# Performance work log

Measured on AMD Instinct MI355X. Metric: run time of the kernel, lower is better.

Reference implementation:

```python
import jax, jax.numpy as jnp
import numpy as np
from jax import lax

B, T, F_IN = 16, 512, 229
CONV = 768      # model_complexity_conv * 16
LSTM_H = 768    # model_complexity_lstm * 16
P = 88          # output_features
NCLS = 5
EMB = 2


def _conv(x, w, b, pad):
    y = lax.conv_general_dilated(x, w, (1, 1), pad,
                                 dimension_numbers=('NCHW', 'OIHW', 'NCHW'))
    return y + b[None, :, None, None]


def _bn(x, g, bta, m, v):
    # eval-mode BatchNorm2d with running stats, eps=1e-5
    s = g * lax.rsqrt(v + 1e-5)
    return x * s[None, :, None, None] + (bta - m * s)[None, :, None, None]


def _pool2w(x):
    # MaxPool2d((1,2))
    return lax.reduce_window(x, -jnp.inf, lax.max, (1, 1, 1, 2), (1, 1, 1, 2), 'VALID')


def _cell(x, h, c, Wih, Whh, bih, bhh):
    # PyTorch LSTM cell, gate order i,f,g,o
    z = x @ Wih.T + h @ Whh.T + bih + bhh
    i, f, g, o = jnp.split(z, 4, axis=-1)
    c = jax.nn.sigmoid(f) * c + jax.nn.sigmoid(i) * jnp.tanh(g)
    h = jax.nn.sigmoid(o) * jnp.tanh(c)
    return h, c


def _forward(mel, c1w, c1b, bn1g, bn1b, bn1m, bn1v,
             c2w, c2b, bn2g, bn2b, bn2m, bn2v,
             c3w, c3b, bn3g, bn3b, bn3m, bn3v,
             fcw, fcb, wih0, whh0, bih0, bhh0,
             wih1, whh1, bih1, bhh1, pw, pb, emb):
    # ---- ConvStack (eval mode: dropout = identity) ----
    x = mel[:, None]                                   # (B,1,T,F)
    x = jax.nn.relu(_bn(_conv(x, c1w, c1b, [(1, 1), (1, 1)]), bn1g, bn1b, bn1m, bn1v))
    x = jax.nn.relu(_bn(_conv(x, c2w, c2b, [(1, 1), (1, 1)]), bn2g, bn2b, bn2m, bn2v))
    x = _pool2w(x)
    x = jax.nn.relu(_bn(_conv(x, c3w, c3b, [(0, 0), (1, 1)]), bn3g, bn3b, bn3m, bn3v))  # time -2
    x = _pool2w(x)                                     # (B, C/8, T-2, F//4)
    x = jnp.transpose(x, (0, 2, 1, 3)).reshape(x.shape[0], x.shape[2], -1)
    acoustic = x @ fcw.T + fcb                         # (B, T-2, CONV)

    Bsz = acoustic.shape[0]
    h1 = jnp.zeros((Bsz, LSTM_H), acoustic.dtype)
    c1 = jnp.zeros((Bsz, LSTM_H), acoustic.dtype)
    h2 = jnp.zeros((Bsz, LSTM_H), acoustic.dtype)
    c2 = jnp.zeros((Bsz, LSTM_H), acoustic.dtype)
    prev = jnp.zeros((Bsz, P * EMB), acoustic.dtype)

    def step(carry, a_t):
        h1, c1, h2, c2, prev = carry
        xt = jnp.concatenate([a_t, prev], axis=-1)     # (B, CONV + 2P)
        h1, c1 = _cell(xt, h1, c1, wih0, whh0, bih0, bhh0)
        h2, c2 = _cell(h1, h2, c2, wih1, whh1, bih1, bhh1)
        logits = (h2 @ pw.T + pb).reshape(Bsz, P, NCLS)
        idx = jnp.argmax(logits, axis=-1)              # argmax(softmax) == argmax(logits)
        prev = emb[idx].reshape(Bsz, P * EMB)
        return (h1, c1, h2, c2, prev), logits

    _, out = lax.scan(step, (h1, c1, h2, c2, prev), jnp.swapaxes(acoustic, 0, 1))
    return jnp.swapaxes(out, 0, 1)                     # (B, T-2, P, 5) raw logits


def setup_inputs() -> dict:
    key = jax.random.key(0)
    ks = iter(jax.random.split(key, 48))

    def rn(shape, s=0.05):
        return jax.random.normal(next(ks), shape, dtype=jnp.float32) * s

    C16, C8 = CONV // 16, CONV // 8
    d = {}
    d['mel'] = jax.random.normal(next(ks), (B, T, F_IN), dtype=jnp.float32)
    d['c1w'] = rn((C16, 1, 3, 3), 0.2); d['c1b'] = rn((C16,))
    d['c2w'] = rn((C16, C16, 3, 3), 0.1); d['c2b'] = rn((C16,))
    d['c3w'] = rn((C8, C16, 3, 3), 0.1); d['c3b'] = rn((C8,))
    for n, ch in (('1', C16), ('2', C16), ('3', C8)):
        d['bn%sg' % n] = jnp.ones((ch,), jnp.float32)
        d['bn%sb' % n] = jnp.zeros((ch,), jnp.float32)
        d['bn%sm' % n] = rn((ch,), 0.1)
        d['bn%sv' % n] = jnp.ones((ch,), jnp.float32)
    d['fcw'] = rn((CONV, C8 * (F_IN // 4)), 0.02); d['fcb'] = rn((CONV,))
    in_l = CONV + P * EMB
    d['wih0'] = rn((4 * LSTM_H, in_l), 0.03); d['whh0'] = rn((4 * LSTM_H, LSTM_H), 0.03)
    d['bih0'] = rn((4 * LSTM_H,)); d['bhh0'] = rn((4 * LSTM_H,))
    d['wih1'] = rn((4 * LSTM_H, LSTM_H), 0.03); d['whh1'] = rn((4 * LSTM_H, LSTM_H), 0.03)
    d['bih1'] = rn((4 * LSTM_H,)); d['bhh1'] = rn((4 * LSTM_H,))
    d['pw'] = rn((P * NCLS, LSTM_H), 0.03); d['pb'] = rn((P * NCLS,))
    d['emb'] = rn((NCLS, EMB), 1.0)
    return d


def reference(mel, c1w, c1b, c2w, c2b, c3w, c3b,
              bn1g, bn1b, bn1m, bn1v, bn2g, bn2b, bn2m, bn2v,
              bn3g, bn3b, bn3m, bn3v, fcw, fcb,
              wih0, whh0, bih0, bhh0, wih1, whh1, bih1, bhh1,
              pw, pb, emb):
    return _forward(mel, c1w, c1b, bn1g, bn1b, bn1m, bn1v,
                    c2w, c2b, bn2g, bn2b, bn2m, bn2v,
                    c3w, c3b, bn3g, bn3b, bn3m, bn3v,
                    fcw, fcb, wih0, whh0, bih0, bhh0,
                    wih1, whh1, bih1, bhh1, pw, pb, emb)
```

## Files before the change

### kernel.cpp

```cpp
#include <hip/hip_runtime.h>
#include <math.h>


typedef unsigned long long ull;

#define ACO_FL 6266880ull
#define F1_OFF 0
#define F2_OFF 3072
#define PC_OFF 6144
#define BAR_U32 8192
#define NCOMP 192
#define NPROJ 44

__device__ __forceinline__ float sigf(float x) { return 1.0f / (1.0f + expf(-x)); }

__device__ __forceinline__ ull pack2(float x, float y) {
  union { float f[2]; ull u; } c; c.f[0] = x; c.f[1] = y; return c.u;
}
__device__ __forceinline__ ull at_load(const ull* p) {
  return __hip_atomic_load((ull*)p, __ATOMIC_RELAXED, __HIP_MEMORY_SCOPE_AGENT);
}
__device__ __forceinline__ void at_store(ull* p, ull v) {
  __hip_atomic_store(p, v, __ATOMIC_RELAXED, __HIP_MEMORY_SCOPE_AGENT);
}

__device__ __forceinline__ void gl2lds(const float4* g, float* l) {
  __builtin_amdgcn_global_load_lds(
      (const __attribute__((address_space(1))) void*)(g),
      (__attribute__((address_space(3))) void*)(l), 16, 0, 17);
}
__device__ __forceinline__ void gl2lds_nc(const float4* g, float* l) {
  __builtin_amdgcn_global_load_lds(
      (const __attribute__((address_space(1))) void*)(g),
      (__attribute__((address_space(3))) void*)(l), 16, 0, 0);
}

__device__ __forceinline__ void wait_flags(const unsigned* f, unsigned tgt, int tid) {
  if (tid < NCOMP) {
    const unsigned* fp = f + tid * 16;
    while (__hip_atomic_load((unsigned*)fp, __ATOMIC_RELAXED,
                             __HIP_MEMORY_SCOPE_AGENT) < tgt)
      __builtin_amdgcn_s_sleep(1);
  }
  __atomic_signal_fence(__ATOMIC_SEQ_CST);
  __syncthreads();
}

__device__ __forceinline__ void pwait(const unsigned* pc, unsigned target) {
  for (;;) {
    unsigned s0 = 0;
#pragma unroll
    for (int i = 0; i < 8; ++i)
      s0 += __hip_atomic_load((unsigned*)(pc + i * 16), __ATOMIC_RELAXED,
                              __HIP_MEMORY_SCOPE_AGENT);
    if (s0 >= target) break;
    __builtin_amdgcn_s_sleep(1);
  }
  __atomic_signal_fence(__ATOMIC_SEQ_CST);
}

__device__ __forceinline__ float red16(float v) {
  v += __shfl_xor(v, 1, 16);
  v += __shfl_xor(v, 2, 16);
  v += __shfl_xor(v, 4, 16);
  v += __shfl_xor(v, 8, 16);
  return v;
}

#define CDOT48(W, PTR, RES) do {                                              \
  const float* _p = (PTR);                                                    \
  float _a0 = 0.f, _a1 = 0.f, _a2 = 0.f, _a3 = 0.f;                           \
  _Pragma("unroll")                                                           \
  for (int _i = 0; _i < 48; _i += 16) {                                       \
    float4 _v0 = *(const float4*)(_p + _i);                                   \
    float4 _v1 = *(const float4*)(_p + _i + 4);                               \
    float4 _v2 = *(const float4*)(_p + _i + 8);                               \
    float4 _v3 = *(const float4*)(_p + _i + 12);                              \
    _a0 = fmaf((W)[_i + 0], _v0.x, _a0); _a0 = fmaf((W)[_i + 1], _v0.y, _a0); \
    _a0 = fmaf((W)[_i + 2], _v0.z, _a0); _a0 = fmaf((W)[_i + 3], _v0.w, _a0); \
    _a1 = fmaf((W)[_i + 4], _v1.x, _a1); _a1 = fmaf((W)[_i + 5], _v1.y, _a1); \
    _a1 = fmaf((W)[_i + 6], _v1.z, _a1); _a1 = fmaf((W)[_i + 7], _v1.w, _a1); \
    _a2 = fmaf((W)[_i + 8], _v2.x, _a2); _a2 = fmaf((W)[_i + 9], _v2.y, _a2); \
    _a2 = fmaf((W)[_i +10], _v2.z, _a2); _a2 = fmaf((W)[_i +11], _v2.w, _a2); \
    _a3 = fmaf((W)[_i +12], _v3.x, _a3); _a3 = fmaf((W)[_i +13], _v3.y, _a3); \
    _a3 = fmaf((W)[_i +14], _v3.z, _a3); _a3 = fmaf((W)[_i +15], _v3.w, _a3); \
  }                                                                           \
  RES = (_a0 + _a1) + (_a2 + _a3);                                            \
} while (0)

#define STAGE_H(SRC, DSTF) do {                                              \
  const float4* _g = (const float4*)(const void*)(SRC);                      \
  _Pragma("unroll")                                                          \
  for (int _cc = 0; _cc < 4; ++_cc) {                                        \
    int _c = wv * 4 + _cc;                                                   \
    _Pragma("unroll")                                                        \
    for (int _k = 0; _k < 3; ++_k)                                           \
      gl2lds(_g + _c * 192 + _k * 64 + ln, (DSTF) + _c * 772 + _k * 256);    \
  }                                                                          \
} while (0)

#define STAGE_PREV(PAR) do {                                                 \
  const float4* _gp = (const float4*)(const void*)(prevg + (size_t)(PAR) * 1408); \
  _Pragma("unroll")                                                          \
  for (int _j = 0; _j < 11; ++_j)                                            \
    if (wv == (_j & 3))                                                      \
      gl2lds(_gp + _j * 64 + ln, prevs + _j * 256);                          \
} while (0)

#define STAGE_X(T) do {                                                      \
  const float4* _gx = (const float4*)(aco + (size_t)(T) * 12288);            \
  _Pragma("unroll")                                                          \
  for (int _cc = 0; _cc < 4; ++_cc) {                                        \
    int _c = wv * 4 + _cc;                                                   \
    _Pragma("unroll")                                                        \
    for (int _k = 0; _k < 3; ++_k) {                                         \
      int _u = _k * 64 + ln;                                                 \
      int _b = _u / 12, _m = _u - _b * 12;                                   \
      gl2lds_nc(_gx + _b * 192 + _c * 12 + _m, bufA + _c * 772 + _k * 256);  \
    }                                                                        \
  }                                                                          \
} while (0)

__global__ __launch_bounds__(256) void conv12_kernel(
    const float* __restrict__ mel,
    const float* __restrict__ c1w, const float* __restrict__ c1b,
    const float* __restrict__ bn1g, const float* __restrict__ bn1b,
    const float* __restrict__ bn1m, const float* __restrict__ bn1v,
    const float* __restrict__ c2w, const float* __restrict__ c2b,
    const float* __restrict__ bn2g, const float* __restrict__ bn2b,
    const float* __restrict__ bn2m, const float* __restrict__ bn2v,
    float* __restrict__ A, int b0)
{
  __shared__ float melS[5 * 232];
  __shared__ float x1S[12 * 3 * 232];
  __shared__ float wS[48 * 12 * 9];
  const int tid = threadIdx.x;
  const int bl = blockIdx.x >> 9;
  const int b = b0 + bl;
  const int t = blockIdx.x & 511;

  for (int idx = tid; idx < 5 * 232; idx += 256) {
    int rr = idx / 232, cc = idx - rr * 232;
    int r = t - 2 + rr, w = cc - 1;
    float v = 0.f;
    if (r >= 0 && r < 512 && w >= 0 && w < 229) v = mel[(b * 512 + r) * 229 + w];
    melS[idx] = v;
  }

  float accA[22], accB[22];
#pragma unroll
  for (int i = 0; i < 22; ++i) { accA[i] = 0.f; accB[i] = 0.f; }
  __syncthreads();

  for (int icc = 0; icc < 4; ++icc) {
    if (icc) __syncthreads();
    for (int idx = tid; idx < 12 * 3 * 232; idx += 256) {
      int cl = idx / (3 * 232);
      int rem = idx - cl * (3 * 232);
      int rr = rem / 232, cc = rem - rr * 232;
      int c = icc * 12 + cl;
      int r1 = t - 1 + rr, w = cc - 1;
      float v = 0.f;
      if (r1 >= 0 && r1 < 512 && w >= 0 && w < 229) {
        const float* cw = c1w + c * 9;
        const float* m0 = melS + rr * 232 + cc - 1;
        float s = m0[0] * cw[0] + m0[1] * cw[1] + m0[2] * cw[2]
                + m0[232] * cw[3] + m0[233] * cw[4] + m0[234] * cw[5]
                + m0[464] * cw[6] + m0[465] * cw[7] + m0[466] * cw[8];
        s += c1b[c];
        float sc = bn1g[c] * rsqrtf(bn1v[c] + 1e-5f);
        v = fmaxf(s * sc + (bn1b[c] - bn1m[c] * sc), 0.f);
      }
      x1S[idx] = v;
    }
    for (int idx = tid; idx < 48 * 12 * 9; idx += 256) {
      int oc = idx / 108, rem = idx - oc * 108;
      wS[idx] = c2w[(oc * 48 + icc * 12) * 9 + rem];
    }
    __syncthreads();
    for (int i = 0; i < 22; ++i) {
      int oidx = tid + i * 256;
      if (oidx >= 5472) break;
      int oc = oidx / 114, wp = oidx - oc * 114;
      int w0 = 2 * wp;
      float a0 = accA[i], a1 = accB[i];
      const float* wp9 = wS + oc * 108;
      for (int icl = 0; icl < 12; ++icl) {
#pragma unroll
        for (int a = 0; a < 3; ++a) {
          const float* xr = x1S + (icl * 3 + a) * 232 + w0;
          float x0 = xr[0], x1 = xr[1], x2 = xr[2], x3 = xr[3];
          float wA = wp9[icl * 9 + a * 3 + 0];
          float wB = wp9[icl * 9 + a * 3 + 1];
          float wC = wp9[icl * 9 + a * 3 + 2];
          a0 = fmaf(x0, wA, a0); a0 = fmaf(x1, wB, a0); a0 = fmaf(x2, wC, a0);
          a1 = fmaf(x1, wA, a1); a1 = fmaf(x2, wB, a1); a1 = fmaf(x3, wC, a1);
        }
      }
      accA[i] = a0; accB[i] = a1;
    }
  }
  for (int i = 0; i < 22; ++i) {
    int oidx = tid + i * 256;
    if (oidx >= 5472) break;
    int oc = oidx / 114, wp = oidx - oc * 114;
    float sc = bn2g[oc] * rsqrtf(bn2v[oc] + 1e-5f);
    float sh = bn2b[oc] - bn2m[oc] * sc;
    float v0 = fmaxf((accA[i] + c2b[oc]) * sc + sh, 0.f);
    float v1 = fmaxf((accB[i] + c2b[oc]) * sc + sh, 0.f);
    A[((bl * 48 + oc) * 512 + t) * 114 + wp] = fmaxf(v0, v1);
  }
}

__global__ __launch_bounds__(256) void conv3_kernel(
    const float* __restrict__ A,
    const float* __restrict__ c3w, const float* __restrict__ c3b,
    const float* __restrict__ bn3g, const float* __restrict__ bn3b,
    const float* __restrict__ bn3m, const float* __restrict__ bn3v,
    float* __restrict__ Bf)
{
  __shared__ float aS[16 * 3 * 116];
  __shared__ float wS[48 * 16 * 9];
  const int tid = threadIdx.x;
  const int bl = blockIdx.x / 510;
  const int t = blockIdx.x - bl * 510;

  for (int ocg = 0; ocg < 2; ++ocg) {
    float accA[11], accB[11];
#pragma unroll
    for (int i = 0; i < 11; ++i) { accA[i] = 0.f; accB[i] = 0.f; }
    for (int icc = 0; icc < 3; ++icc) {
      __syncthreads();
      for (int idx = tid; idx < 16 * 3 * 116; idx += 256) {
        int cl = idx / 348, rem = idx - cl * 348;
        int rr = rem / 116, cc = rem - rr * 116;
        int w = cc - 1;
        float v = 0.f;
        if (w >= 0 && w < 114) v = A[((bl * 48 + icc * 16 + cl) * 512 + t + rr) * 114 + w];
        aS[idx] = v;
      }
      for (int idx = tid; idx < 48 * 16 * 9; idx += 256) {
        int ocl = idx / 144, rem = idx - ocl * 144;
        wS[idx] = c3w[((ocg * 48 + ocl) * 48 + icc * 16) * 9 + rem];
      }
      __syncthreads();
      for (int i = 0; i < 11; ++i) {
        int oidx = tid + i * 256;
        if (oidx >= 2736) break;
        int ocl = oidx / 57, wp = oidx - ocl * 57;
        int w0 = 2 * wp;
        float a0 = accA[i], a1 = accB[i];
        const float* wb = wS + ocl * 144;
        for (int icl = 0; icl < 16; ++icl) {
#pragma unroll
          for (int a = 0; a < 3; ++a) {
            const float* xr = aS + (icl * 3 + a) * 116 + w0;
            float x0 = xr[0], x1 = xr[1], x2 = xr[2], x3 = xr[3];
            float wA = wb[icl * 9 + a * 3 + 0];
            float wB = wb[icl * 9 + a * 3 + 1];
            float wC = wb[icl * 9 + a * 3 + 2];
            a0 = fmaf(x0, wA, a0); a0 = fmaf(x1, wB, a0); a0 = fmaf(x2, wC, a0);
            a1 = fmaf(x1, wA, a1); a1 = fmaf(x2, wB, a1); a1 = fmaf(x3, wC, a1);
          }
        }
        accA[i] = a0; accB[i] = a1;
      }
    }
    for (int i = 0; i < 11; ++i) {
      int oidx = tid + i * 256;
      if (oidx >= 2736) break;
      int ocl = oidx / 57, wp = oidx - ocl * 57;
      int oc = ocg * 48 + ocl;
      float sc = bn3g[oc] * rsqrtf(bn3v[oc] + 1e-5f);
      float sh = bn3b[oc] - bn3m[oc] * sc;
      float v0 = fmaxf((accA[i] + c3b[oc]) * sc + sh, 0.f);
      float v1 = fmaxf((accB[i] + c3b[oc]) * sc + sh, 0.f);
      Bf[(size_t)(bl * 510 + t) * 5472 + oc * 57 + wp] = fmaxf(v0, v1);
    }
  }
}

__global__ __launch_bounds__(256) void gemm_nt(
    const float* __restrict__ Am, const float* __restrict__ Bm,
    const float* __restrict__ bias, float* __restrict__ C,
    int M, int K, int lda, int ldb, int b0)
{
  __shared__ float As[64 * 33];
  __shared__ float Bs[64 * 33];
  const int tid = threadIdx.x;
  const int m0 = blockIdx.x * 64, n0 = blockIdx.y * 64;
  const int tx = tid & 15, ty = tid >> 4;
  const int kq = (tid & 7) * 4, rw = tid >> 3;
  float acc[4][4];
#pragma unroll
  for (int i = 0; i < 4; ++i)
#pragma unroll
    for (int j = 0; j < 4; ++j) acc[i][j] = 0.f;

  for (int k0 = 0; k0 < K; k0 += 32) {
    int m1 = m0 + rw, m2 = m1 + 32;
    float4 va = make_float4(0.f, 0.f, 0.f, 0.f), vb = va;
    if (m1 < M) va = *(const float4*)(Am + (size_t)m1 * lda + k0 + kq);
    if (m2 < M) vb = *(const float4*)(Am + (size_t)m2 * lda + k0 + kq);
    float4 wa = *(const float4*)(Bm + (size_t)(n0 + rw) * ldb + k0 + kq);
    float4 wb = *(const float4*)(Bm + (size_t)(n0 + rw + 32) * ldb + k0 + kq);
    As[rw * 33 + kq + 0] = va.x; As[rw * 33 + kq + 1] = va.y;
    As[rw * 33 + kq + 2] = va.z; As[rw * 33 + kq + 3] = va.w;
    As[(rw + 32) * 33 + kq + 0] = vb.x; As[(rw + 32) * 33 + kq + 1] = vb.y;
    As[(rw + 32) * 33 + kq + 2] = vb.z; As[(rw + 32) * 33 + kq + 3] = vb.w;
    Bs[rw * 33 + kq + 0] = wa.x; Bs[rw * 33 + kq + 1] = wa.y;
    Bs[rw * 33 + kq + 2] = wa.z; Bs[rw * 33 + kq + 3] = wa.w;
    Bs[(rw + 32) * 33 + kq + 0] = wb.x; Bs[(rw + 32) * 33 + kq + 1] = wb.y;
    Bs[(rw + 32) * 33 + kq + 2] = wb.z; Bs[(rw + 32) * 33 + kq + 3] = wb.w;
    __syncthreads();
#pragma unroll 8
    for (int k = 0; k < 32; ++k) {
      float av[4], bv[4];
#pragma unroll
      for (int i = 0; i < 4; ++i) av[i] = As[(ty * 4 + i) * 33 + k];
#pragma unroll
      for (int j = 0; j < 4; ++j) bv[j] = Bs[(tx * 4 + j) * 33 + k];
#pragma unroll
      for (int i = 0; i < 4; ++i)
#pragma unroll
        for (int j = 0; j < 4; ++j) acc[i][j] = fmaf(av[i], bv[j], acc[i][j]);
    }
    __syncthreads();
  }
#pragma unroll
  for (int i = 0; i < 4; ++i) {
    int m = m0 + ty * 4 + i;
    if (m >= M) continue;
    int bl2 = m / 510, tt2 = m - bl2 * 510;
    float* crow = C + ((size_t)tt2 * 16 + (b0 + bl2)) * 768;
#pragma unroll
    for (int j = 0; j < 4; ++j) {
      int n = n0 + tx * 4 + j;
      crow[n] = acc[i][j] + bias[n];
    }
  }
}

__global__ void init_state(ull* __restrict__ h1g, ull* __restrict__ h2g,
                           ull* __restrict__ prevg, unsigned* __restrict__ bar) {
  int gid = blockIdx.x * 256 + threadIdx.x;
  if (gid < 12288) { at_store(h1g + gid, 0ull); at_store(h2g + gid, 0ull); }
  if (gid < 2816) at_store(prevg + gid, 0ull);
  if (gid < BAR_U32)
    __hip_atomic_store(bar + gid, 0u, __ATOMIC_RELAXED, __HIP_MEMORY_SCOPE_AGENT);
}

__global__ __launch_bounds__(256, 1) void lstm_kernel(
    const float* __restrict__ aco,
    const float* __restrict__ whh0,
    const float* __restrict__ wih0,
    const float* __restrict__ wih1,
    const float* __restrict__ whh1,
    const float* __restrict__ bih0, const float* __restrict__ bhh0,
    const float* __restrict__ bih1, const float* __restrict__ bhh1,
    const float* __restrict__ pw,
    const float* __restrict__ pb,
    const float* __restrict__ emb,
    ull* __restrict__ h1g,
    ull* __restrict__ h2g,
    ull* __restrict__ prevg,
    unsigned* __restrict__ bar,
    float* __restrict__ out)
{
  __shared__ float bufA[16 * 772];
  __shared__ float bufB[16 * 772];
  __shared__ float bufC[16 * 772];
  __shared__ float prevs[16 * 176];
  __shared__ float zl[16 * 17];
  __shared__ float harr[64];
  __shared__ float embS[10];
  const int tid = threadIdx.x;
  const int s = tid & 15;
  const int r = tid >> 4;
  const int wv = tid >> 6;
  const int ln = tid & 63;
  unsigned* f1 = bar + F1_OFF;
  unsigned* f2 = bar + F2_OFF;
  unsigned* pc = bar + PC_OFF;

  if (blockIdx.x < NCOMP) {
    const int uB = blockIdx.x * 4;
    const int j = (r >> 2) * 768 + uB + (r & 3);

    float wx[48], w0[48], w1[48], w2[48], wp[11];
    {
      const float* p = wih0 + (size_t)j * 944 + 48 * s;
#pragma unroll
      for (int i = 0; i < 48; i += 4) {
        float4 v = *(const float4*)(p + i);
        wx[i] = v.x; wx[i+1] = v.y; wx[i+2] = v.z; wx[i+3] = v.w;
      }
      p = whh0 + (size_t)j * 768 + 48 * s;
#pragma unroll
      for (int i = 0; i < 48; i += 4) {
        float4 v = *(const float4*)(p + i);
        w0[i] = v.x; w0[i+1] = v.y; w0[i+2] = v.z; w0[i+3] = v.w;
      }
      p = wih1 + (size_t)j * 768 + 48 * s;
#pragma unroll
      for (int i = 0; i < 48; i += 4) {
        float4 v = *(const float4*)(p + i);
        w1[i] = v.x; w1[i+1] = v.y; w1[i+2] = v.z; w1[i+3] = v.w;
      }
      p = whh1 + (size_t)j * 768 + 48 * s;
#pragma unroll
      for (int i = 0; i < 48; i += 4) {
        float4 v = *(const float4*)(p + i);
        w2[i] = v.x; w2[i+1] = v.y; w2[i+2] = v.z; w2[i+3] = v.w;
      }
      const float* pp = wih0 + (size_t)j * 944 + 768 + 11 * s;
#pragma unroll
      for (int i = 0; i < 11; ++i) wp[i] = pp[i];
    }
    float bl1[4], bl2[4], c1 = 0.f, c2 = 0.f;
    if (tid < 64) {
      int ul = tid >> 4;
#pragma unroll
      for (int g = 0; g < 4; ++g) {
        int jj = g * 768 + uB + ul;
        bl1[g] = bih0[jj] + bhh0[jj];
        bl2[g] = bih1[jj] + bhh1[jj];
      }
    }
    const int hdst = (blockIdx.x / 12) * 384 + (blockIdx.x % 12) * 2;

    for (int i = tid; i < 16 * 772; i += 256) { bufB[i] = 0.f; bufC[i] = 0.f; }

    float zxr[16];
    STAGE_X(0);
    __syncthreads();
#pragma unroll 4
    for (int b = 0; b < 16; ++b) {
      float p; CDOT48(wx, bufA + s * 772 + b * 48, p);
      zxr[b] = red16(p);
    }

    for (int t = 0; t < 510; ++t) {
      const int wbuf = t & 1, rbuf = wbuf ^ 1;
      __syncthreads();
#pragma unroll 4
      for (int b = 0; b < 16; ++b) {
        float p; CDOT48(w0, bufB + s * 772 + b * 48, p);
        p = red16(p);
        if (s == 0) zl[r * 17 + b] = zxr[b] + p;
      }
      if (tid == 0 && t) pwait(pc, (unsigned)(NPROJ * t));
      __syncthreads();
      STAGE_H(h2g + rbuf * 6144, bufC);
      STAGE_PREV(rbuf);
      __syncthreads();
#pragma unroll 4
      for (int b = 0; b < 16; ++b) {
        const float* pvv = prevs + b * 176 + s * 11;
        float p = 0.f;
#pragma unroll
        for (int i = 0; i < 11; ++i) p = fmaf(wp[i], pvv[i], p);
        p = red16(p);
        if (s == 0) zl[r * 17 + b] += p;
      }
      __syncthreads();
      if (tid < 64) {
        int ul = tid >> 4, bb = tid & 15;
        float zi = zl[(0 * 4 + ul) * 17 + bb] + bl1[0];
        float zf = zl[(1 * 4 + ul) * 17 + bb] + bl1[1];
        float zg = zl[(2 * 4 + ul) * 17 + bb] + bl1[2];
        float zo = zl[(3 * 4 + ul) * 17 + bb] + bl1[3];
        c1 = sigf(zf) * c1 + sigf(zi) * tanhf(zg);
        harr[tid] = sigf(zo) * tanhf(c1);
      }
      __syncthreads();
      if (tid < 32) {
        int q = tid >> 4, bb = tid & 15;
        at_store(h1g + wbuf * 6144 + hdst + bb * 24 + q,
                 pack2(harr[(2 * q) * 16 + bb], harr[(2 * q + 1) * 16 + bb]));
      }
      if (tid == 0) {
        __builtin_amdgcn_s_waitcnt(0);
        __atomic_signal_fence(__ATOMIC_SEQ_CST);
        __hip_atomic_store(f1 + blockIdx.x * 16, (unsigned)(t + 1),
                           __ATOMIC_RELAXED, __HIP_MEMORY_SCOPE_AGENT);
      }
      if (t < 509) {
        STAGE_X(t + 1);
        __syncthreads();
#pragma unroll 4
        for (int b = 0; b < 16; ++b) {
          float p; CDOT48(wx, bufA + s * 772 + b * 48, p);
          zxr[b] = red16(p);
        }
      }
      wait_flags(f1, (unsigned)(t + 1), tid);
      STAGE_H(h1g + wbuf * 6144, bufB);
      __syncthreads();
#pragma unroll 2
      for (int b = 0; b < 16; ++b) {
        float p1, p2;
        CDOT48(w1, bufB + s * 772 + b * 48, p1);
        CDOT48(w2, bufC + s * 772 + b * 48, p2);
        float p = red16(p1 + p2);
        if (s == 0) zl[r * 17 + b] = p;
      }
      __syncthreads();
      if (tid < 64) {
        int ul = tid >> 4, bb = tid & 15;
        float zi = zl[(0 * 4 + ul) * 17 + bb] + bl2[0];
        float zf = zl[(1 * 4 + ul) * 17 + bb] + bl2[1];
        float zg = zl[(2 * 4 + ul) * 17 + bb] + bl2[2];
        float zo = zl[(3 * 4 + ul) * 17 + bb] + bl2[3];
        c2 = sigf(zf) * c2 + sigf(zi) * tanhf(zg);
        harr[tid] = sigf(zo) * tanhf(c2);
      }
      __syncthreads();
      if (tid < 32) {
        int q = tid >> 4, bb = tid & 15;
        at_store(h2g + wbuf * 6144 + hdst + bb * 24 + q,
                 pack2(harr[(2 * q) * 16 + bb], harr[(2 * q + 1) * 16 + bb]));
      }
      if (tid == 0) {
        __builtin_amdgcn_s_waitcnt(0);
        __atomic_signal_fence(__ATOMIC_SEQ_CST);
        __hip_atomic_store(f2 + blockIdx.x * 16, (unsigned)(t + 1),
                           __ATOMIC_RELAXED, __HIP_MEMORY_SCOPE_AGENT);
      }
    }
  } else {
    const int bp = blockIdx.x - NCOMP;
    const int prow = bp * 10 + r;
    float pwr[48];
    float pbv = 0.f;
    if (r < 10) {
      const float* p = pw + (size_t)prow * 768 + 48 * s;
#pragma unroll
      for (int i = 0; i < 48; i += 4) {
        float4 v = *(const float4*)(p + i);
        pwr[i] = v.x; pwr[i+1] = v.y; pwr[i+2] = v.z; pwr[i+3] = v.w;
      }
      pbv = pb[prow];
    } else {
#pragma unroll
      for (int i = 0; i < 48; ++i) pwr[i] = 0.f;
    }
    if (tid < 10) embS[tid] = emb[tid];
    __syncthreads();

    for (int t = 0; t < 510; ++t) {
      const int wbuf = t & 1;
      wait_flags(f2, (unsigned)(t + 1), tid);
      STAGE_H(h2g + wbuf * 6144, bufA);
      __syncthreads();
#pragma unroll 4
      for (int b = 0; b < 16; ++b) {
        float p; CDOT48(pwr, bufA + s * 772 + b * 48, p);
        p = red16(p);
        if (r < 10 && s == 0) {
          float lg = p + pbv;
          out[((size_t)b * 510 + t) * 440 + prow] = lg;
          zl[r * 17 + b] = lg;
        }
      }
      __syncthreads();
      if (tid < 32) {
        int q = tid >> 4, bb = tid & 15;
        float best = zl[(q * 5) * 17 + bb]; int bi = 0;
#pragma unroll
        for (int c = 1; c < 5; ++c) {
          float v = zl[(q * 5 + c) * 17 + bb];
          if (v > best) { best = v; bi = c; }
        }
        at_store(prevg + wbuf * 1408 + bb * 88 + bp * 2 + q,
                 pack2(embS[bi * 2], embS[bi * 2 + 1]));
      }
      __syncthreads();
      if (tid == 0) {
        __builtin_amdgcn_s_waitcnt(0);
        __atomic_signal_fence(__ATOMIC_SEQ_CST);
        __hip_atomic_fetch_add(pc + (bp & 7) * 16, 1u,
                               __ATOMIC_RELAXED, __HIP_MEMORY_SCOPE_AGENT);
      }
    }
  }
}

extern "C" void kernel_launch(void* const* d_in, const int* in_sizes, int n_in,
                              void* d_out, int out_size, void* d_ws, size_t ws_size,
                              hipStream_t stream) {
  (void)in_sizes; (void)n_in; (void)out_size;
  const float* mel  = (const float*)d_in[0];
  const float* c1w  = (const float*)d_in[1];
  const float* c1b  = (const float*)d_in[2];
  const float* c2w  = (const float*)d_in[3];
  const float* c2b  = (const float*)d_in[4];
  const float* c3w  = (const float*)d_in[5];
  const float* c3b  = (const float*)d_in[6];
  const float* bn1g = (const float*)d_in[7];
  const float* bn1b = (const float*)d_in[8];
  const float* bn1m = (const float*)d_in[9];
  const float* bn1v = (const float*)d_in[10];
  const float* bn2g = (const float*)d_in[11];
  const float* bn2b = (const float*)d_in[12];
  const float* bn2m = (const float*)d_in[13];
  const float* bn2v = (const float*)d_in[14];
  const float* bn3g = (const float*)d_in[15];
  const float* bn3b = (const float*)d_in[16];
  const float* bn3m = (const float*)d_in[17];
  const float* bn3v = (const float*)d_in[18];
  const float* fcw  = (const float*)d_in[19];
  const float* fcb  = (const float*)d_in[20];
  const float* wih0 = (const float*)d_in[21];
  const float* whh0 = (const float*)d_in[22];
  const float* bih0 = (const float*)d_in[23];
  const float* bhh0 = (const float*)d_in[24];
  const float* wih1 = (const float*)d_in[25];
  const float* whh1 = (const float*)d_in[26];
  const float* bih1 = (const float*)d_in[27];
  const float* bhh1 = (const float*)d_in[28];
  const float* pw   = (const float*)d_in[29];
  const float* pb   = (const float*)d_in[30];
  const float* emb  = (const float*)d_in[31];

  float* ws = (float*)d_ws;
  float* outp = (float*)d_out;

  const size_t ST_ULL = 12288ull + 12288ull + 2816ull;
  int CB = 1;
  for (int cb = 4; cb >= 1; cb >>= 1) {
    size_t need = (ACO_FL + (size_t)cb * 48 * 512 * 114 + (size_t)cb * 510 * 5472) * 4
                + ST_ULL * 8 + BAR_U32 * 4 + 1024;
    if (ws_size >= need) { CB = cb; break; }
  }
  const int nchunks = 16 / CB;
  const size_t A_FL  = (size_t)CB * 48 * 512 * 114;
  const size_t BF_FL = (size_t)CB * 510 * 5472;

  float* aco = ws;
  float* Ac  = ws + ACO_FL;
  float* Bfc = Ac + A_FL;
  ull* h1g   = (ull*)(Bfc + BF_FL);
  ull* h2g   = h1g + 12288;
  ull* prevg = h2g + 12288;
  unsigned* bar = (unsigned*)(prevg + 2816);

  for (int ch = 0; ch < nchunks; ++ch) {
    int b0 = ch * CB;
    hipLaunchKernelGGL(conv12_kernel, dim3(CB * 512), dim3(256), 0, stream,
                       mel, c1w, c1b, bn1g, bn1b, bn1m, bn1v,
                       c2w, c2b, bn2g, bn2b, bn2m, bn2v, Ac, b0);
    hipLaunchKernelGGL(conv3_kernel, dim3(CB * 510), dim3(256), 0, stream,
                       Ac, c3w, c3b, bn3g, bn3b, bn3m, bn3v, Bfc);
    int M = CB * 510;
    hipLaunchKernelGGL(gemm_nt, dim3((M + 63) / 64, 12), dim3(256), 0, stream,
                       Bfc, fcw, fcb, aco, M, 5472, 5472, 5472, b0);
  }
  hipLaunchKernelGGL(init_state, dim3(48), dim3(256), 0, stream,
                     h1g, h2g, prevg, bar);

  {
    void* args[] = {
      (void*)&aco, (void*)&whh0, (void*)&wih0, (void*)&wih1, (void*)&whh1,
      (void*)&bih0, (void*)&bhh0, (void*)&bih1, (void*)&bhh1,
      (void*)&pw, (void*)&pb, (void*)&emb,
      (void*)&h1g, (void*)&h2g, (void*)&prevg, (void*)&bar, (void*)&outp
    };
    hipError_t e = hipLaunchCooperativeKernel((const void*)lstm_kernel,
                                              dim3(NCOMP + NPROJ), dim3(256),
                                              args, 0, stream);
    if (e != hipSuccess) {
      (void)hipGetLastError();
      hipLaunchKernelGGL(lstm_kernel, dim3(NCOMP + NPROJ), dim3(256), 0, stream,
                         aco, whh0, wih0, wih1, whh1, bih0, bhh0, bih1, bhh1,
                         pw, pb, emb, h1g, h2g, prevg, bar, outp);
    }
  }
}
```

Before: 25.84 ms.

## Replace projection counter barrier with per-block flags and trim syncthreads

The projection blocks now each publish their own step counter, and the compute blocks poll these flags in parallel across threads instead of one thread summing eight atomically incremented counters. The gate outputs are exchanged by wavefront shuffles rather than through a shared array, which removes a block barrier per layer. The next-step x staging is issued earlier so it overlaps the recurrent dot products, and the sleep interval while polling goes from 1 to 4. The changes aim to shorten the per-timestep critical path of the 510-step serial decode. They also relax ordering: one barrier in the projection blocks is dropped, and the earlier staging of x writes into bufA, so correctness depends on the remaining barriers still ordering those accesses.

Result: faster. 24.84 ms (-3.9%).

```diff
diff --git a/kernel.cpp b/kernel.cpp
--- a/kernel.cpp
+++ b/kernel.cpp
@@ -7,7 +7,7 @@
 #define ACO_FL 6266880ull
 #define F1_OFF 0
 #define F2_OFF 3072
-#define PC_OFF 6144
+#define FP_OFF 6144
 #define BAR_U32 8192
 #define NCOMP 192
 #define NPROJ 44
@@ -35,28 +35,20 @@
       (__attribute__((address_space(3))) void*)(l), 16, 0, 0);
 }
 
-__device__ __forceinline__ void wait_flags(const unsigned* f, unsigned tgt, int tid) {
-  if (tid < NCOMP) {
+__device__ __forceinline__ void wait_flags_n(const unsigned* f, unsigned tgt,
+                                             int tid, int n) {
+  if (tid < n) {
     const unsigned* fp = f + tid * 16;
-    while (__hip_atomic_load((unsigned*)fp, __ATOMIC_RELAXED,
-                             __HIP_MEMORY_SCOPE_AGENT) < tgt)
-      __builtin_amdgcn_s_sleep(1);
+    unsigned v = __hip_atomic_load((unsigned*)fp, __ATOMIC_RELAXED,
+                                   __HIP_MEMORY_SCOPE_AGENT);
+    while (v < tgt) {
+      __builtin_amdgcn_s_sleep(4);
+      v = __hip_atomic_load((unsigned*)fp, __ATOMIC_RELAXED,
+                            __HIP_MEMORY_SCOPE_AGENT);
+    }
   }
   __atomic_signal_fence(__ATOMIC_SEQ_CST);
   __syncthreads();
-}
-
-__device__ __forceinline__ void pwait(const unsigned* pc, unsigned target) {
-  for (;;) {
-    unsigned s0 = 0;
-#pragma unroll
-    for (int i = 0; i < 8; ++i)
-      s0 += __hip_atomic_load((unsigned*)(pc + i * 16), __ATOMIC_RELAXED,
-                              __HIP_MEMORY_SCOPE_AGENT);
-    if (s0 >= target) break;
-    __builtin_amdgcn_s_sleep(1);
-  }
-  __atomic_signal_fence(__ATOMIC_SEQ_CST);
 }
 
 __device__ __forceinline__ float red16(float v) {
@@ -372,7 +364,6 @@
   __shared__ float bufC[16 * 772];
   __shared__ float prevs[16 * 176];
   __shared__ float zl[16 * 17];
-  __shared__ float harr[64];
   __shared__ float embS[10];
   const int tid = threadIdx.x;
   const int s = tid & 15;
@@ -381,7 +372,7 @@
   const int ln = tid & 63;
   unsigned* f1 = bar + F1_OFF;
   unsigned* f2 = bar + F2_OFF;
-  unsigned* pc = bar + PC_OFF;
+  unsigned* fp = bar + FP_OFF;
 
   if (blockIdx.x < NCOMP) {
     const int uB = blockIdx.x * 4;
@@ -443,14 +434,15 @@
     for (int t = 0; t < 510; ++t) {
       const int wbuf = t & 1, rbuf = wbuf ^ 1;
       __syncthreads();
+      if (t < 509) STAGE_X(t + 1);
 #pragma unroll 4
       for (int b = 0; b < 16; ++b) {
         float p; CDOT48(w0, bufB + s * 772 + b * 48, p);
         p = red16(p);
         if (s == 0) zl[r * 17 + b] = zxr[b] + p;
       }
-      if (tid == 0 && t) pwait(pc, (unsigned)(NPROJ * t));
-      __syncthreads();
+      if (t) wait_flags_n(fp, (unsigned)t, tid, NPROJ);
+      else __syncthreads();
       STAGE_H(h2g + rbuf * 6144, bufC);
       STAGE_PREV(rbuf);
       __syncthreads();
@@ -471,30 +463,29 @@
         float zg = zl[(2 * 4 + ul) * 17 + bb] + bl1[2];
         float zo = zl[(3 * 4 + ul) * 17 + bb] + bl1[3];
         c1 = sigf(zf) * c1 + sigf(zi) * tanhf(zg);
-        harr[tid] = sigf(zo) * tanhf(c1);
-      }
-      __syncthreads();
-      if (tid < 32) {
-        int q = tid >> 4, bb = tid & 15;
-        at_store(h1g + wbuf * 6144 + hdst + bb * 24 + q,
-                 pack2(harr[(2 * q) * 16 + bb], harr[(2 * q + 1) * 16 + bb]));
-      }
-      if (tid == 0) {
-        __builtin_amdgcn_s_waitcnt(0);
-        __atomic_signal_fence(__ATOMIC_SEQ_CST);
-        __hip_atomic_store(f1 + blockIdx.x * 16, (unsigned)(t + 1),
-                           __ATOMIC_RELAXED, __HIP_MEMORY_SCOPE_AGENT);
+        float h = sigf(zo) * tanhf(c1);
+        int src1 = (tid >> 4) * 32 + (tid & 15);
+        float v1 = __shfl(h, src1, 64);
+        float v2 = __shfl(h, src1 + 16, 64);
+        if (tid < 32) {
+          int q = tid >> 4, bb2 = tid & 15;
+          at_store(h1g + wbuf * 6144 + hdst + bb2 * 24 + q, pack2(v1, v2));
+        }
+        if (tid == 0) {
+          __builtin_amdgcn_s_waitcnt(0);
+          __atomic_signal_fence(__ATOMIC_SEQ_CST);
+          __hip_atomic_store(f1 + blockIdx.x * 16, (unsigned)(t + 1),
+                             __ATOMIC_RELAXED, __HIP_MEMORY_SCOPE_AGENT);
+        }
       }
       if (t < 509) {
-        STAGE_X(t + 1);
-        __syncthreads();
 #pragma unroll 4
         for (int b = 0; b < 16; ++b) {
           float p; CDOT48(wx, bufA + s * 772 + b * 48, p);
           zxr[b] = red16(p);
         }
       }
-      wait_flags(f1, (unsigned)(t + 1), tid);
+      wait_flags_n(f1, (unsigned)(t + 1), tid, NCOMP);
       STAGE_H(h1g + wbuf * 6144, bufB);
       __syncthreads();
 #pragma unroll 2
@@ -513,19 +504,20 @@
         float zg = zl[(2 * 4 + ul) * 17 + bb] + bl2[2];
         float zo = zl[(3 * 4 + ul) * 17 + bb] + bl2[3];
         c2 = sigf(zf) * c2 + sigf(zi) * tanhf(zg);
-        harr[tid] = sigf(zo) * tanhf(c2);
-      }
-      __syncthreads();
-      if (tid < 32) {
-        int q = tid >> 4, bb = tid & 15;
-        at_store(h2g + wbuf * 6144 + hdst + bb * 24 + q,
-                 pack2(harr[(2 * q) * 16 + bb], harr[(2 * q + 1) * 16 + bb]));
-      }
-      if (tid == 0) {
-        __builtin_amdgcn_s_waitcnt(0);
-        __atomic_signal_fence(__ATOMIC_SEQ_CST);
-        __hip_atomic_store(f2 + blockIdx.x * 16, (unsigned)(t + 1),
-                           __ATOMIC_RELAXED, __HIP_MEMORY_SCOPE_AGENT);
+        float h = sigf(zo) * tanhf(c2);
+        int src1 = (tid >> 4) * 32 + (tid & 15);
+        float v1 = __shfl(h, src1, 64);
+        float v2 = __shfl(h, src1 + 16, 64);
+        if (tid < 32) {
+          int q = tid >> 4, bb2 = tid & 15;
+          at_store(h2g + wbuf * 6144 + hdst + bb2 * 24 + q, pack2(v1, v2));
+        }
+        if (tid == 0) {
+          __builtin_amdgcn_s_waitcnt(0);
+          __atomic_signal_fence(__ATOMIC_SEQ_CST);
+          __hip_atomic_store(f2 + blockIdx.x * 16, (unsigned)(t + 1),
+                             __ATOMIC_RELAXED, __HIP_MEMORY_SCOPE_AGENT);
+        }
       }
     }
   } else {
@@ -550,7 +542,7 @@
 
     for (int t = 0; t < 510; ++t) {
       const int wbuf = t & 1;
-      wait_flags(f2, (unsigned)(t + 1), tid);
+      wait_flags_n(f2, (unsigned)(t + 1), tid, NCOMP);
       STAGE_H(h2g + wbuf * 6144, bufA);
       __syncthreads();
 #pragma unroll 4
@@ -575,12 +567,11 @@
         at_store(prevg + wbuf * 1408 + bb * 88 + bp * 2 + q,
                  pack2(embS[bi * 2], embS[bi * 2 + 1]));
       }
-      __syncthreads();
       if (tid == 0) {
         __builtin_amdgcn_s_waitcnt(0);
         __atomic_signal_fence(__ATOMIC_SEQ_CST);
-        __hip_atomic_fetch_add(pc + (bp & 7) * 16, 1u,
-                               __ATOMIC_RELAXED, __HIP_MEMORY_SCOPE_AGENT);
+        __hip_atomic_store(fp + bp * 16, (unsigned)(t + 1),
+                           __ATOMIC_RELAXED, __HIP_MEMORY_SCOPE_AGENT);
       }
     }
   }
```
